# Kernel optimization log

Measured on AMD Instinct MI355X. Metric: run time of the kernel, lower is better.

Reference implementation:

```python
import jax, jax.numpy as jnp
import numpy as np

E = 8       # num experts
D = 768     # embed_dim
H = 12      # num heads
F = 3072    # expert hidden = 4*D
TOPK = 2


def setup_inputs() -> dict:
    key = jax.random.key(0)
    ks = jax.random.split(key, 8)
    B, S = 4, 1024
    s = lambda d: 1.0 / np.sqrt(d)
    return {
        "x": jax.random.normal(ks[0], (B, S, D), jnp.float32),
        "w_qkv": jax.random.normal(ks[1], (D, 3 * D), jnp.float32) * s(D),
        "b_qkv": jnp.zeros((3 * D,), jnp.float32),
        "w_o": jax.random.normal(ks[2], (D, D), jnp.float32) * s(D),
        "b_o": jnp.zeros((D,), jnp.float32),
        "w_router": jax.random.normal(ks[3], (D, E), jnp.float32) * s(D),
        "w1": jax.random.normal(ks[4], (E, D, F), jnp.float32) * s(D),
        "b1": jnp.zeros((E, F), jnp.float32),
        "w2": jax.random.normal(ks[5], (E, F, D), jnp.float32) * s(F),
        "b2": jnp.zeros((E, D), jnp.float32),
    }


def reference(x, w_qkv, b_qkv, w_o, b_o, w_router, w1, b1, w2, b2):
    B, S, Dm = x.shape
    hd = Dm // H
    # --- multi-head self-attention ---
    qkv = x @ w_qkv + b_qkv                                  # [B,S,3D]
    q, k, v = jnp.split(qkv, 3, axis=-1)
    resh = lambda t: t.reshape(B, S, H, hd).transpose(0, 2, 1, 3)  # [B,H,S,hd]
    q, k, v = resh(q), resh(k), resh(v)
    scores = jnp.einsum('bhqd,bhkd->bhqk', q, k) / np.sqrt(hd).astype(np.float32)
    attn = jax.nn.softmax(scores, axis=-1)
    ctx = jnp.einsum('bhqk,bhkd->bhqd', attn, v)
    ctx = ctx.transpose(0, 2, 1, 3).reshape(B, S, Dm)
    y = ctx @ w_o + b_o                                      # [B,S,D]
    # --- top-k MoE feed-forward ---
    t = y.reshape(B * S, Dm)                                 # [T,D]
    logits = t @ w_router                                    # [T,E]
    probs = jax.nn.softmax(logits, axis=-1)
    topv, topi = jax.lax.top_k(probs, TOPK)                  # [T,K]
    topw = topv / jnp.sum(topv, axis=-1, keepdims=True)      # renormalized gates
    T = t.shape[0]
    wfull = jnp.zeros_like(probs).at[jnp.arange(T)[:, None], topi].set(topw)  # [T,E]
    # dense all-expert compute, weighted combine (faithful to routed math)
    h = jax.nn.gelu(jnp.einsum('td,edf->etf', t, w1) + b1[:, None, :])  # [E,T,F]
    oe = jnp.einsum('etf,efd->etd', h, w2) + b2[:, None, :]              # [E,T,D]
    out = jnp.einsum('te,etd->td', wfull, oe).reshape(B, S, Dm)
    diagnostics = probs  # router probabilities as diagnostics
    return (out, diagnostics)
```

## Files before the change

### kernel.cpp

```cpp
#include <hip/hip_runtime.h>
#include <hip/hip_bf16.h>
#include <cstdint>
#include <cmath>

#define T_TOK 4096
#define DIM   768
#define HEADS 12
#define HD    64
#define NEXP  8
#define FDIM  3072

typedef __attribute__((ext_vector_type(8))) short short8v;
typedef __attribute__((ext_vector_type(4))) float float4v;

__device__ __forceinline__ float gelu_tanh(float x) {
  float u = 0.7978845608028654f * (x + 0.044715f * x * x * x);
  return 0.5f * x * (1.0f + tanhf(u));
}

__device__ __forceinline__ short f2bf(float x) {
  __hip_bfloat16 h = __float2bfloat16(x);
  return *reinterpret_cast<short*>(&h);
}

template<int TBM, int TBN>
__global__ __launch_bounds__(256) void gemm_f32(
    const float* __restrict__ A, const float* __restrict__ W,
    const float* __restrict__ bias, float* __restrict__ C,
    int M, int N, int K)
{
  constexpr int MM = TBM / 16;
  constexpr int MN = TBN / 16;
  constexpr int ALOAD = TBM * 16 / 256;
  constexpr int BLOAD = TBN * 16 / 256;
  __shared__ float As[16][TBM + 4];
  __shared__ float Bs[16][TBN + 4];
  const int bm = blockIdx.y * TBM;
  const int bn = blockIdx.x * TBN;
  const int tid = threadIdx.x;
  const int tr = tid >> 4;
  const int tc = tid & 15;

  float acc[MM][MN] = {};

  for (int k0 = 0; k0 < K; k0 += 16) {
    #pragma unroll
    for (int i = 0; i < ALOAD; i++) {
      int idx = tid + i * 256;
      int m  = idx >> 4;
      int kk = idx & 15;
      As[kk][m] = A[(size_t)(bm + m) * K + k0 + kk];
    }
    #pragma unroll
    for (int i = 0; i < BLOAD; i++) {
      int idx = tid + i * 256;
      int kk = idx / TBN;
      int n  = idx % TBN;
      Bs[kk][n] = W[(size_t)(k0 + kk) * N + bn + n];
    }
    __syncthreads();
    #pragma unroll
    for (int kk = 0; kk < 16; kk++) {
      float a[MM], b[MN];
      #pragma unroll
      for (int u4 = 0; u4 < MM / 4; u4++) {
        float4 t = *(const float4*)&As[kk][tr * MM + u4 * 4];
        a[u4*4+0]=t.x; a[u4*4+1]=t.y; a[u4*4+2]=t.z; a[u4*4+3]=t.w;
      }
      #pragma unroll
      for (int v4 = 0; v4 < MN / 4; v4++) {
        float4 t = *(const float4*)&Bs[kk][tc * MN + v4 * 4];
        b[v4*4+0]=t.x; b[v4*4+1]=t.y; b[v4*4+2]=t.z; b[v4*4+3]=t.w;
      }
      #pragma unroll
      for (int u = 0; u < MM; u++)
        #pragma unroll
        for (int v = 0; v < MN; v++)
          acc[u][v] = fmaf(a[u], b[v], acc[u][v]);
    }
    __syncthreads();
  }

  #pragma unroll
  for (int u = 0; u < MM; u++) {
    int row = bm + tr * MM + u;
    #pragma unroll
    for (int v4 = 0; v4 < MN / 4; v4++) {
      int col = bn + tc * MN + v4 * 4;
      float4 o;
      o.x = acc[u][v4*4+0] + bias[col+0];
      o.y = acc[u][v4*4+1] + bias[col+1];
      o.z = acc[u][v4*4+2] + bias[col+2];
      o.w = acc[u][v4*4+3] + bias[col+3];
      *(float4*)&C[(size_t)row * N + col] = o;
    }
  }
}

__global__ __launch_bounds__(256) void transpose_bf16(
    const float* __restrict__ W, short* __restrict__ WT, int K, int N)
{
  __shared__ float t[32][33];
  const size_t mat = (size_t)K * N;
  const float* Wp = W + blockIdx.z * mat;
  short* WTp = WT + blockIdx.z * mat;
  int n0 = blockIdx.x * 32, k0 = blockIdx.y * 32;
  int tx = threadIdx.x, ty = threadIdx.y;
  #pragma unroll
  for (int i = 0; i < 4; i++)
    t[ty + i * 8][tx] = Wp[(size_t)(k0 + ty + i * 8) * N + n0 + tx];
  __syncthreads();
  #pragma unroll
  for (int i = 0; i < 4; i++)
    WTp[(size_t)(n0 + ty + i * 8) * K + k0 + tx] = f2bf(t[tx][ty + i * 8]);
}

__global__ __launch_bounds__(256) void y2bf_kernel(
    const float* __restrict__ y, short* __restrict__ ybf)
{
  int g = blockIdx.x * 256 + threadIdx.x;
  float4 v = *(const float4*)&y[(size_t)g * 4];
  short4 s = make_short4(f2bf(v.x), f2bf(v.y), f2bf(v.z), f2bf(v.w));
  *(short4*)&ybf[(size_t)g * 4] = s;
}

__global__ __launch_bounds__(256) void moe_up(
    const short* __restrict__ ybf, const short* __restrict__ WT,
    const float* __restrict__ bias, short* __restrict__ hbuf,
    const int* __restrict__ offsets, const int* __restrict__ perm)
{
  const int e = blockIdx.z;
  const int start = offsets[e];
  const int M = offsets[e + 1] - start;
  const int bm = blockIdx.y * 128;
  if (bm >= M) return;
  const int bn = blockIdx.x * 128;

  __shared__ short As[4][128][8];
  __shared__ short Bs[4][128][8];
  __shared__ int   perm_s[128];

  const int tid  = threadIdx.x;
  const int lane = tid & 63;
  const int wave = tid >> 6;
  const int wm = wave >> 1, wn = wave & 1;
  const int lr = lane & 15;
  const int kb = lane >> 4;

  const short* WTe = WT + (size_t)e * ((size_t)FDIM * DIM);
  const float* be  = bias + (size_t)e * FDIM;

  if (tid < 128) {
    int rr = bm + tid;
    perm_s[tid] = (rr < M) ? perm[start + rr] : perm[start];
  }
  __syncthreads();

  const int q = tid & 3;
  const int mrow = tid >> 2;
  const short* aptr[2];
  const short* bptr[2];
  #pragma unroll
  for (int i = 0; i < 2; i++) {
    aptr[i] = ybf + (size_t)perm_s[mrow + i * 64] * DIM;
    bptr[i] = WTe + (size_t)(bn + mrow + i * 64) * DIM;
  }

  float4v acc[4][4] = {};

  for (int k0 = 0; k0 < DIM; k0 += 32) {
    int4 av[2], bv[2];
    #pragma unroll
    for (int i = 0; i < 2; i++) {
      av[i] = *(const int4*)(aptr[i] + k0 + q * 8);
      bv[i] = *(const int4*)(bptr[i] + k0 + q * 8);
    }
    __syncthreads();
    #pragma unroll
    for (int i = 0; i < 2; i++) {
      *(int4*)&As[q][mrow + i * 64][0] = av[i];
      *(int4*)&Bs[q][mrow + i * 64][0] = bv[i];
    }
    __syncthreads();

    short8v af[4], bfv[4];
    #pragma unroll
    for (int mi = 0; mi < 4; mi++)
      af[mi] = *(const short8v*)&As[kb][wm * 64 + mi * 16 + lr][0];
    #pragma unroll
    for (int ni = 0; ni < 4; ni++)
      bfv[ni] = *(const short8v*)&Bs[kb][wn * 64 + ni * 16 + lr][0];
    #pragma unroll
    for (int mi = 0; mi < 4; mi++)
      #pragma unroll
      for (int ni = 0; ni < 4; ni++)
        acc[mi][ni] = __builtin_amdgcn_mfma_f32_16x16x32_bf16(
            af[mi], bfv[ni], acc[mi][ni], 0, 0, 0);
  }

  #pragma unroll
  for (int ni = 0; ni < 4; ni++) {
    int col = bn + wn * 64 + ni * 16 + lr;
    float b = be[col];
    #pragma unroll
    for (int mi = 0; mi < 4; mi++) {
      int lrow0 = wm * 64 + mi * 16 + kb * 4;
      #pragma unroll
      for (int r = 0; r < 4; r++) {
        int rr = bm + lrow0 + r;
        if (rr < M)
          hbuf[(size_t)(start + rr) * FDIM + col] = f2bf(gelu_tanh(acc[mi][ni][r] + b));
      }
    }
  }
}

__global__ __launch_bounds__(256) void moe_down(
    const short* __restrict__ hbuf, const short* __restrict__ WT,
    const float* __restrict__ bias, float* __restrict__ oe,
    const int* __restrict__ offsets)
{
  const int e = blockIdx.z;
  const int start = offsets[e];
  const int M = offsets[e + 1] - start;
  const int bm = blockIdx.y * 64;
  if (bm >= M) return;
  const int bn = blockIdx.x * 128;

  __shared__ short As[4][64][8];
  __shared__ short Bs[4][128][8];

  const int tid  = threadIdx.x;
  const int lane = tid & 63;
  const int wn   = tid >> 6;
  const int lr   = lane & 15;
  const int kb   = lane >> 4;

  const short* WTe = WT + (size_t)e * ((size_t)DIM * FDIM);
  const float* be  = bias + (size_t)e * DIM;

  const int q = tid & 3;
  const int mrow = tid >> 2;
  int rr0 = bm + mrow; if (rr0 >= M) rr0 = M - 1;
  const short* aptr = hbuf + (size_t)(start + rr0) * FDIM;
  const short* bptr[2];
  #pragma unroll
  for (int i = 0; i < 2; i++)
    bptr[i] = WTe + (size_t)(bn + mrow + i * 64) * FDIM;

  float4v acc[4][2] = {};

  for (int k0 = 0; k0 < FDIM; k0 += 32) {
    int4 av = *(const int4*)(aptr + k0 + q * 8);
    int4 bv[2];
    #pragma unroll
    for (int i = 0; i < 2; i++) bv[i] = *(const int4*)(bptr[i] + k0 + q * 8);
    __syncthreads();
    *(int4*)&As[q][mrow][0] = av;
    #pragma unroll
    for (int i = 0; i < 2; i++) *(int4*)&Bs[q][mrow + i * 64][0] = bv[i];
    __syncthreads();

    short8v af[4], bfv[2];
    #pragma unroll
    for (int mi = 0; mi < 4; mi++)
      af[mi] = *(const short8v*)&As[kb][mi * 16 + lr][0];
    #pragma unroll
    for (int ni = 0; ni < 2; ni++)
      bfv[ni] = *(const short8v*)&Bs[kb][wn * 32 + ni * 16 + lr][0];
    #pragma unroll
    for (int mi = 0; mi < 4; mi++)
      #pragma unroll
      for (int ni = 0; ni < 2; ni++)
        acc[mi][ni] = __builtin_amdgcn_mfma_f32_16x16x32_bf16(
            af[mi], bfv[ni], acc[mi][ni], 0, 0, 0);
  }

  #pragma unroll
  for (int ni = 0; ni < 2; ni++) {
    int col = bn + wn * 32 + ni * 16 + lr;
    float b = be[col];
    #pragma unroll
    for (int mi = 0; mi < 4; mi++) {
      #pragma unroll
      for (int r = 0; r < 4; r++) {
        int rr = bm + mi * 16 + kb * 4 + r;
        if (rr < M)
          oe[(size_t)(start + rr) * DIM + col] = acc[mi][ni][r] + b;
      }
    }
  }
}

__global__ __launch_bounds__(256) void combine_kernel(
    const float* __restrict__ oe, const int* __restrict__ ppos,
    const float* __restrict__ topg, float* __restrict__ out)
{
  int g = blockIdx.x * 256 + threadIdx.x;
  int t = g / 192;
  int c = (g - t * 192) * 4;
  int p0 = ppos[2 * t], p1 = ppos[2 * t + 1];
  float g0 = topg[2 * t], g1 = topg[2 * t + 1];
  float4 a = *(const float4*)&oe[(size_t)p0 * DIM + c];
  float4 b = *(const float4*)&oe[(size_t)p1 * DIM + c];
  float4 o;
  o.x = g0 * a.x + g1 * b.x;
  o.y = g0 * a.y + g1 * b.y;
  o.z = g0 * a.z + g1 * b.z;
  o.w = g0 * a.w + g1 * b.w;
  *(float4*)&out[(size_t)t * DIM + c] = o;
}

__global__ __launch_bounds__(256) void attn_kernel(
    const float* __restrict__ qkv, float* __restrict__ ctx)
{
  const int qt = blockIdx.x;
  const int bh = blockIdx.y;
  const int b = bh / HEADS, h = bh % HEADS;
  const float* base = qkv + (size_t)b * 1024 * (3 * DIM) + h * 64;

  __shared__ float ks[64][64];
  __shared__ float vs[64][64];

  const int tid   = threadIdx.x;
  const int wv    = tid >> 6;
  const int qhalf = wv & 1;
  const int khalf = wv >> 1;
  const int lane  = tid & 63;
  const int grp   = lane >> 2;
  const int sub   = lane & 3;
  const int q0    = qhalf * 32 + grp * 2;
  const int dpart = sub * 16;

  const float qscale = 0.125f * 1.44269504088896f;
  float qA[16], qB[16], accA[16] = {}, accB[16] = {};
  float lA = 0.f, lB = 0.f;

  {
    const float* qpA = base + (size_t)(qt * 64 + q0) * (3 * DIM) + dpart;
    const float* qpB = qpA + 3 * DIM;
    #pragma unroll
    for (int d4 = 0; d4 < 4; d4++) {
      float4 ta = *(const float4*)(qpA + d4 * 4);
      float4 tb = *(const float4*)(qpB + d4 * 4);
      qA[d4*4+0]=ta.x*qscale; qA[d4*4+1]=ta.y*qscale; qA[d4*4+2]=ta.z*qscale; qA[d4*4+3]=ta.w*qscale;
      qB[d4*4+0]=tb.x*qscale; qB[d4*4+1]=tb.y*qscale; qB[d4*4+2]=tb.z*qscale; qB[d4*4+3]=tb.w*qscale;
    }
  }

  for (int kt = 0; kt < 16; kt++) {
    __syncthreads();
    #pragma unroll
    for (int i = 0; i < 4; i++) {
      int idx = tid + i * 256;
      int r = idx >> 4, c4 = idx & 15;
      const float* kp = base + (size_t)(kt * 64 + r) * (3 * DIM) + c4 * 4;
      *(float4*)&ks[r][c4 * 4] = *(const float4*)(kp + DIM);
      *(float4*)&vs[r][c4 * 4] = *(const float4*)(kp + 2 * DIM);
    }
    __syncthreads();

    #pragma unroll 2
    for (int jj = 0; jj < 32; jj++) {
      int j = khalf * 32 + jj;
      float4 k0v = *(const float4*)&ks[j][dpart];
      float4 k1v = *(const float4*)&ks[j][dpart + 4];
      float4 k2v = *(const float4*)&ks[j][dpart + 8];
      float4 k3v = *(const float4*)&ks[j][dpart + 12];
      float kr[16] = {k0v.x,k0v.y,k0v.z,k0v.w, k1v.x,k1v.y,k1v.z,k1v.w,
                      k2v.x,k2v.y,k2v.z,k2v.w, k3v.x,k3v.y,k3v.z,k3v.w};
      float sA = 0.f, sB = 0.f;
      #pragma unroll
      for (int d = 0; d < 16; d++) {
        sA = fmaf(qA[d], kr[d], sA);
        sB = fmaf(qB[d], kr[d], sB);
      }
      sA += __shfl_xor(sA, 1);  sB += __shfl_xor(sB, 1);
      sA += __shfl_xor(sA, 2);  sB += __shfl_xor(sB, 2);
      float pA = exp2f(sA);
      float pB = exp2f(sB);
      lA += pA;  lB += pB;
      float4 v0v = *(const float4*)&vs[j][dpart];
      float4 v1v = *(const float4*)&vs[j][dpart + 4];
      float4 v2v = *(const float4*)&vs[j][dpart + 8];
      float4 v3v = *(const float4*)&vs[j][dpart + 12];
      float vr[16] = {v0v.x,v0v.y,v0v.z,v0v.w, v1v.x,v1v.y,v1v.z,v1v.w,
                      v2v.x,v2v.y,v2v.z,v2v.w, v3v.x,v3v.y,v3v.z,v3v.w};
      #pragma unroll
      for (int d = 0; d < 16; d++) {
        accA[d] = fmaf(pA, vr[d], accA[d]);
        accB[d] = fmaf(pB, vr[d], accB[d]);
      }
    }
  }

  __syncthreads();
  if (khalf == 1) {
    #pragma unroll
    for (int d4 = 0; d4 < 4; d4++) {
      *(float4*)&ks[q0][dpart + d4*4] =
          make_float4(accA[d4*4], accA[d4*4+1], accA[d4*4+2], accA[d4*4+3]);
      *(float4*)&ks[q0 + 1][dpart + d4*4] =
          make_float4(accB[d4*4], accB[d4*4+1], accB[d4*4+2], accB[d4*4+3]);
    }
    if (sub == 0) { vs[0][q0] = lA; vs[0][q0 + 1] = lB; }
  }
  __syncthreads();
  if (khalf == 0) {
    lA += vs[0][q0];
    lB += vs[0][q0 + 1];
    float invA = 1.f / lA, invB = 1.f / lB;
    float* opA = ctx + ((size_t)b * 1024 + qt * 64 + q0) * DIM + h * 64 + dpart;
    float* opB = opA + DIM;
    #pragma unroll
    for (int d4 = 0; d4 < 4; d4++) {
      float4 ca = *(const float4*)&ks[q0][dpart + d4*4];
      float4 cb = *(const float4*)&ks[q0 + 1][dpart + d4*4];
      float4 oa, ob;
      oa.x = (accA[d4*4+0] + ca.x) * invA;
      oa.y = (accA[d4*4+1] + ca.y) * invA;
      oa.z = (accA[d4*4+2] + ca.z) * invA;
      oa.w = (accA[d4*4+3] + ca.w) * invA;
      ob.x = (accB[d4*4+0] + cb.x) * invB;
      ob.y = (accB[d4*4+1] + cb.y) * invB;
      ob.z = (accB[d4*4+2] + cb.z) * invB;
      ob.w = (accB[d4*4+3] + cb.w) * invB;
      *(float4*)(opA + d4 * 4) = oa;
      *(float4*)(opB + d4 * 4) = ob;
    }
  }
}

__global__ __launch_bounds__(256) void router_kernel(
    const float* __restrict__ y, const float* __restrict__ wr,
    float* __restrict__ probs, int* __restrict__ topi,
    float* __restrict__ topg, int* __restrict__ counts)
{
  __shared__ float w[DIM * NEXP];
  const int tid = threadIdx.x;
  for (int i = tid; i < DIM * NEXP; i += 256) w[i] = wr[i];
  __syncthreads();

  const int t = blockIdx.x * 256 + tid;
  const float* yp = y + (size_t)t * DIM;
  float logit[8] = {};
  for (int d = 0; d < DIM; d++) {
    float xv = yp[d];
    #pragma unroll
    for (int e = 0; e < 8; e++) logit[e] = fmaf(xv, w[d * 8 + e], logit[e]);
  }
  float mx = logit[0];
  #pragma unroll
  for (int e = 1; e < 8; e++) mx = fmaxf(mx, logit[e]);
  float p[8], sum = 0.f;
  #pragma unroll
  for (int e = 0; e < 8; e++) { p[e] = __expf(logit[e] - mx); sum += p[e]; }
  float inv = 1.f / sum;
  #pragma unroll
  for (int e = 0; e < 8; e++) { p[e] *= inv; probs[(size_t)t * 8 + e] = p[e]; }

  int i0 = 0;
  #pragma unroll
  for (int e = 1; e < 8; e++) if (p[e] > p[i0]) i0 = e;
  int i1 = (i0 == 0) ? 1 : 0;
  #pragma unroll
  for (int e = 0; e < 8; e++) if (e != i0 && p[e] > p[i1]) i1 = e;
  float g = p[i0] + p[i1];
  topi[2 * t] = i0;  topi[2 * t + 1] = i1;
  topg[2 * t] = p[i0] / g;  topg[2 * t + 1] = p[i1] / g;
  atomicAdd(&counts[i0], 1);
  atomicAdd(&counts[i1], 1);
}

__global__ void init_meta(int* counts) {
  if (threadIdx.x < 8) counts[threadIdx.x] = 0;
}

__global__ void scan_kernel(const int* __restrict__ counts,
                            int* __restrict__ offsets, int* __restrict__ cursors) {
  if (threadIdx.x == 0) {
    int s = 0;
    for (int e = 0; e < 8; e++) { offsets[e] = s; cursors[e] = s; s += counts[e]; }
    offsets[8] = s;
  }
}

__global__ __launch_bounds__(256) void scatter_kernel(
    const int* __restrict__ topi, int* __restrict__ cursors,
    int* __restrict__ perm, int* __restrict__ ppos)
{
  const int t = blockIdx.x * 256 + threadIdx.x;
  #pragma unroll
  for (int s = 0; s < 2; s++) {
    int e = topi[2 * t + s];
    int pos = atomicAdd(&cursors[e], 1);
    perm[pos] = t;
    ppos[2 * t + s] = pos;
  }
}

extern "C" void kernel_launch(void* const* d_in, const int* in_sizes, int n_in,
                              void* d_out, int out_size, void* d_ws, size_t ws_size,
                              hipStream_t stream) {
  const float* x        = (const float*)d_in[0];
  const float* w_qkv    = (const float*)d_in[1];
  const float* b_qkv    = (const float*)d_in[2];
  const float* w_o      = (const float*)d_in[3];
  const float* b_o      = (const float*)d_in[4];
  const float* w_router = (const float*)d_in[5];
  const float* w1       = (const float*)d_in[6];
  const float* b1       = (const float*)d_in[7];
  const float* w2       = (const float*)d_in[8];
  const float* b2       = (const float*)d_in[9];

  float* out   = (float*)d_out;
  float* probs = out + (size_t)T_TOK * DIM;

  char* ws = (char*)d_ws;
  float* qkv  = (float*)ws;
  short* hbuf = (short*)ws;
  short* wT   = (short*)(ws + 50331648);
  float* ctx  = (float*)(ws + 88080384);
  short* ybf  = (short*)(ws + 88080384);
  float* oe   = (float*)(ws + 88080384);
  float* y    = (float*)(ws + 100663296);
  char*  meta = ws + 113246208;
  int*   counts  = (int*)meta;
  int*   cursors = counts + 8;
  int*   offsets = cursors + 8;
  int*   topi    = offsets + 16;
  float* topg    = (float*)(topi + 8192);
  int*   perm    = (int*)(topg + 8192);
  int*   ppos    = perm + 8192;

  init_meta<<<1, 64, 0, stream>>>(counts);

  gemm_f32<128, 64><<<dim3((3 * DIM) / 64, T_TOK / 128), 256, 0, stream>>>(
      x, w_qkv, b_qkv, qkv, T_TOK, 3 * DIM, DIM);

  attn_kernel<<<dim3(16, 48), 256, 0, stream>>>(qkv, ctx);

  gemm_f32<64, 64><<<dim3(DIM / 64, T_TOK / 64), 256, 0, stream>>>(
      ctx, w_o, b_o, y, T_TOK, DIM, DIM);

  router_kernel<<<16, 256, 0, stream>>>(y, w_router, probs, topi, topg, counts);
  scan_kernel<<<1, 64, 0, stream>>>(counts, offsets, cursors);
  scatter_kernel<<<16, 256, 0, stream>>>(topi, cursors, perm, ppos);

  y2bf_kernel<<<(T_TOK * DIM / 4) / 256, 256, 0, stream>>>(y, ybf);

  transpose_bf16<<<dim3(FDIM / 32, DIM / 32, NEXP), dim3(32, 8), 0, stream>>>(
      w1, wT, DIM, FDIM);
  moe_up<<<dim3(FDIM / 128, T_TOK / 128, NEXP), 256, 0, stream>>>(
      ybf, wT, b1, hbuf, offsets, perm);

  transpose_bf16<<<dim3(DIM / 32, FDIM / 32, NEXP), dim3(32, 8), 0, stream>>>(
      w2, wT, FDIM, DIM);
  moe_down<<<dim3(DIM / 128, T_TOK / 64, NEXP), 256, 0, stream>>>(
      hbuf, wT, b2, oe, offsets);

  combine_kernel<<<(T_TOK * DIM / 4) / 256, 256, 0, stream>>>(oe, ppos, topg, out);
}
```

Before: 1.138 ms.

## Register-prefetch next tiles in fp32 GEMM and attention, retile attention threads

The fp32 GEMM now loads A and W tiles as float4 into registers one k-step ahead and stores them to shared memory before computing, dropping one barrier per iteration. The attention kernel likewise prefetches the next K/V tile into registers and remaps threads so each handles 4 queries over 8 head dims, trading extra shuffles for more reuse of each K/V value loaded from shared memory. The QKV GEMM tile grows to 128x128 and launch bounds request 3 blocks per SM. The aim is to hide global-load latency and cut shared-memory traffic per FMA, at the cost of more registers, which could spill or lower occupancy.

```diff
diff --git a/kernel.cpp b/kernel.cpp
--- a/kernel.cpp
+++ b/kernel.cpp
@@ -24,15 +24,15 @@
 }
 
 template<int TBM, int TBN>
-__global__ __launch_bounds__(256) void gemm_f32(
+__global__ __launch_bounds__(256, 3) void gemm_f32(
     const float* __restrict__ A, const float* __restrict__ W,
     const float* __restrict__ bias, float* __restrict__ C,
     int M, int N, int K)
 {
   constexpr int MM = TBM / 16;
   constexpr int MN = TBN / 16;
-  constexpr int ALOAD = TBM * 16 / 256;
-  constexpr int BLOAD = TBN * 16 / 256;
+  constexpr int ALOADS = TBM * 4 / 256;
+  constexpr int BLOADS = TBN * 4 / 256;
   __shared__ float As[16][TBM + 4];
   __shared__ float Bs[16][TBN + 4];
   const int bm = blockIdx.y * TBM;
@@ -42,21 +42,51 @@
   const int tc = tid & 15;
 
   float acc[MM][MN] = {};
+  float4 areg[ALOADS], breg[BLOADS];
+
+  #pragma unroll
+  for (int i = 0; i < ALOADS; i++) {
+    int fidx = tid + i * 256;
+    int row = fidx >> 2, c4 = fidx & 3;
+    areg[i] = *(const float4*)&A[(size_t)(bm + row) * K + c4 * 4];
+  }
+  #pragma unroll
+  for (int i = 0; i < BLOADS; i++) {
+    int fidx = tid + i * 256;
+    int kk = fidx / (TBN / 4), n4 = fidx % (TBN / 4);
+    breg[i] = *(const float4*)&W[(size_t)kk * N + bn + n4 * 4];
+  }
 
   for (int k0 = 0; k0 < K; k0 += 16) {
-    #pragma unroll
-    for (int i = 0; i < ALOAD; i++) {
-      int idx = tid + i * 256;
-      int m  = idx >> 4;
-      int kk = idx & 15;
-      As[kk][m] = A[(size_t)(bm + m) * K + k0 + kk];
-    }
-    #pragma unroll
-    for (int i = 0; i < BLOAD; i++) {
-      int idx = tid + i * 256;
-      int kk = idx / TBN;
-      int n  = idx % TBN;
-      Bs[kk][n] = W[(size_t)(k0 + kk) * N + bn + n];
+    __syncthreads();
+    #pragma unroll
+    for (int i = 0; i < ALOADS; i++) {
+      int fidx = tid + i * 256;
+      int row = fidx >> 2, c4 = fidx & 3;
+      As[c4 * 4 + 0][row] = areg[i].x;
+      As[c4 * 4 + 1][row] = areg[i].y;
+      As[c4 * 4 + 2][row] = areg[i].z;
+      As[c4 * 4 + 3][row] = areg[i].w;
+    }
+    #pragma unroll
+    for (int i = 0; i < BLOADS; i++) {
+      int fidx = tid + i * 256;
+      int kk = fidx / (TBN / 4), n4 = fidx % (TBN / 4);
+      *(float4*)&Bs[kk][n4 * 4] = breg[i];
+    }
+    if (k0 + 16 < K) {
+      #pragma unroll
+      for (int i = 0; i < ALOADS; i++) {
+        int fidx = tid + i * 256;
+        int row = fidx >> 2, c4 = fidx & 3;
+        areg[i] = *(const float4*)&A[(size_t)(bm + row) * K + k0 + 16 + c4 * 4];
+      }
+      #pragma unroll
+      for (int i = 0; i < BLOADS; i++) {
+        int fidx = tid + i * 256;
+        int kk = fidx / (TBN / 4), n4 = fidx % (TBN / 4);
+        breg[i] = *(const float4*)&W[(size_t)(k0 + 16 + kk) * N + bn + n4 * 4];
+      }
     }
     __syncthreads();
     #pragma unroll
@@ -78,7 +108,6 @@
         for (int v = 0; v < MN; v++)
           acc[u][v] = fmaf(a[u], b[v], acc[u][v]);
     }
-    __syncthreads();
   }
 
   #pragma unroll
@@ -311,7 +340,7 @@
   *(float4*)&out[(size_t)t * DIM + c] = o;
 }
 
-__global__ __launch_bounds__(256) void attn_kernel(
+__global__ __launch_bounds__(256, 3) void attn_kernel(
     const float* __restrict__ qkv, float* __restrict__ ctx)
 {
   const int qt = blockIdx.x;
@@ -319,33 +348,40 @@
   const int b = bh / HEADS, h = bh % HEADS;
   const float* base = qkv + (size_t)b * 1024 * (3 * DIM) + h * 64;
 
-  __shared__ float ks[64][64];
-  __shared__ float vs[64][64];
+  __shared__ float ks[64 * 64];
+  __shared__ float vs[64 * 64];
+  __shared__ float lred[2][32];
 
   const int tid   = threadIdx.x;
   const int wv    = tid >> 6;
   const int qhalf = wv & 1;
   const int khalf = wv >> 1;
   const int lane  = tid & 63;
-  const int grp   = lane >> 2;
-  const int sub   = lane & 3;
-  const int q0    = qhalf * 32 + grp * 2;
-  const int dpart = sub * 16;
+  const int grp   = lane >> 3;
+  const int sub   = lane & 7;
+  const int dpart = sub * 8;
+  const int qbase = qhalf * 32 + grp * 4;
 
   const float qscale = 0.125f * 1.44269504088896f;
-  float qA[16], qB[16], accA[16] = {}, accB[16] = {};
-  float lA = 0.f, lB = 0.f;
-
-  {
-    const float* qpA = base + (size_t)(qt * 64 + q0) * (3 * DIM) + dpart;
-    const float* qpB = qpA + 3 * DIM;
-    #pragma unroll
-    for (int d4 = 0; d4 < 4; d4++) {
-      float4 ta = *(const float4*)(qpA + d4 * 4);
-      float4 tb = *(const float4*)(qpB + d4 * 4);
-      qA[d4*4+0]=ta.x*qscale; qA[d4*4+1]=ta.y*qscale; qA[d4*4+2]=ta.z*qscale; qA[d4*4+3]=ta.w*qscale;
-      qB[d4*4+0]=tb.x*qscale; qB[d4*4+1]=tb.y*qscale; qB[d4*4+2]=tb.z*qscale; qB[d4*4+3]=tb.w*qscale;
-    }
+  float q[4][8], acc[4][8] = {}, l[4] = {0.f, 0.f, 0.f, 0.f};
+
+  #pragma unroll
+  for (int i = 0; i < 4; i++) {
+    const float* qp = base + (size_t)(qt * 64 + qbase + i) * (3 * DIM) + dpart;
+    float4 t0 = *(const float4*)qp;
+    float4 t1 = *(const float4*)(qp + 4);
+    q[i][0]=t0.x*qscale; q[i][1]=t0.y*qscale; q[i][2]=t0.z*qscale; q[i][3]=t0.w*qscale;
+    q[i][4]=t1.x*qscale; q[i][5]=t1.y*qscale; q[i][6]=t1.z*qscale; q[i][7]=t1.w*qscale;
+  }
+
+  float4 kreg[4], vreg[4];
+  #pragma unroll
+  for (int i = 0; i < 4; i++) {
+    int idx = tid + i * 256;
+    int r = idx >> 4, c4 = idx & 15;
+    const float* kp = base + (size_t)r * (3 * DIM) + c4 * 4;
+    kreg[i] = *(const float4*)(kp + DIM);
+    vreg[i] = *(const float4*)(kp + 2 * DIM);
   }
 
   for (int kt = 0; kt < 16; kt++) {
@@ -354,79 +390,98 @@
     for (int i = 0; i < 4; i++) {
       int idx = tid + i * 256;
       int r = idx >> 4, c4 = idx & 15;
-      const float* kp = base + (size_t)(kt * 64 + r) * (3 * DIM) + c4 * 4;
-      *(float4*)&ks[r][c4 * 4] = *(const float4*)(kp + DIM);
-      *(float4*)&vs[r][c4 * 4] = *(const float4*)(kp + 2 * DIM);
+      *(float4*)&ks[r * 64 + c4 * 4] = kreg[i];
+      *(float4*)&vs[r * 64 + c4 * 4] = vreg[i];
+    }
+    if (kt < 15) {
+      #pragma unroll
+      for (int i = 0; i < 4; i++) {
+        int idx = tid + i * 256;
+        int r = idx >> 4, c4 = idx & 15;
+        const float* kp = base + (size_t)((kt + 1) * 64 + r) * (3 * DIM) + c4 * 4;
+        kreg[i] = *(const float4*)(kp + DIM);
+        vreg[i] = *(const float4*)(kp + 2 * DIM);
+      }
     }
     __syncthreads();
 
     #pragma unroll 2
     for (int jj = 0; jj < 32; jj++) {
       int j = khalf * 32 + jj;
-      float4 k0v = *(const float4*)&ks[j][dpart];
-      float4 k1v = *(const float4*)&ks[j][dpart + 4];
-      float4 k2v = *(const float4*)&ks[j][dpart + 8];
-      float4 k3v = *(const float4*)&ks[j][dpart + 12];
-      float kr[16] = {k0v.x,k0v.y,k0v.z,k0v.w, k1v.x,k1v.y,k1v.z,k1v.w,
-                      k2v.x,k2v.y,k2v.z,k2v.w, k3v.x,k3v.y,k3v.z,k3v.w};
-      float sA = 0.f, sB = 0.f;
-      #pragma unroll
-      for (int d = 0; d < 16; d++) {
-        sA = fmaf(qA[d], kr[d], sA);
-        sB = fmaf(qB[d], kr[d], sB);
-      }
-      sA += __shfl_xor(sA, 1);  sB += __shfl_xor(sB, 1);
-      sA += __shfl_xor(sA, 2);  sB += __shfl_xor(sB, 2);
-      float pA = exp2f(sA);
-      float pB = exp2f(sB);
-      lA += pA;  lB += pB;
-      float4 v0v = *(const float4*)&vs[j][dpart];
-      float4 v1v = *(const float4*)&vs[j][dpart + 4];
-      float4 v2v = *(const float4*)&vs[j][dpart + 8];
-      float4 v3v = *(const float4*)&vs[j][dpart + 12];
-      float vr[16] = {v0v.x,v0v.y,v0v.z,v0v.w, v1v.x,v1v.y,v1v.z,v1v.w,
-                      v2v.x,v2v.y,v2v.z,v2v.w, v3v.x,v3v.y,v3v.z,v3v.w};
-      #pragma unroll
-      for (int d = 0; d < 16; d++) {
-        accA[d] = fmaf(pA, vr[d], accA[d]);
-        accB[d] = fmaf(pB, vr[d], accB[d]);
+      float4 k0v = *(const float4*)&ks[j * 64 + dpart];
+      float4 k1v = *(const float4*)&ks[j * 64 + dpart + 4];
+      float kr[8] = {k0v.x,k0v.y,k0v.z,k0v.w, k1v.x,k1v.y,k1v.z,k1v.w};
+      float s0 = 0.f, s1 = 0.f, s2 = 0.f, s3 = 0.f;
+      #pragma unroll
+      for (int d = 0; d < 8; d++) {
+        s0 = fmaf(q[0][d], kr[d], s0);
+        s1 = fmaf(q[1][d], kr[d], s1);
+        s2 = fmaf(q[2][d], kr[d], s2);
+        s3 = fmaf(q[3][d], kr[d], s3);
+      }
+      s0 += __shfl_xor(s0, 1); s1 += __shfl_xor(s1, 1);
+      s2 += __shfl_xor(s2, 1); s3 += __shfl_xor(s3, 1);
+      s0 += __shfl_xor(s0, 2); s1 += __shfl_xor(s1, 2);
+      s2 += __shfl_xor(s2, 2); s3 += __shfl_xor(s3, 2);
+      s0 += __shfl_xor(s0, 4); s1 += __shfl_xor(s1, 4);
+      s2 += __shfl_xor(s2, 4); s3 += __shfl_xor(s3, 4);
+      float p0 = exp2f(s0), p1 = exp2f(s1), p2 = exp2f(s2), p3 = exp2f(s3);
+      l[0] += p0; l[1] += p1; l[2] += p2; l[3] += p3;
+      float4 v0v = *(const float4*)&vs[j * 64 + dpart];
+      float4 v1v = *(const float4*)&vs[j * 64 + dpart + 4];
+      float vr[8] = {v0v.x,v0v.y,v0v.z,v0v.w, v1v.x,v1v.y,v1v.z,v1v.w};
+      #pragma unroll
+      for (int d = 0; d < 8; d++) {
+        acc[0][d] = fmaf(p0, vr[d], acc[0][d]);
+        acc[1][d] = fmaf(p1, vr[d], acc[1][d]);
+        acc[2][d] = fmaf(p2, vr[d], acc[2][d]);
+        acc[3][d] = fmaf(p3, vr[d], acc[3][d]);
       }
     }
   }
 
   __syncthreads();
+  float* bufA = ks;
+  float* bufB = vs;
   if (khalf == 1) {
-    #pragma unroll
-    for (int d4 = 0; d4 < 4; d4++) {
-      *(float4*)&ks[q0][dpart + d4*4] =
-          make_float4(accA[d4*4], accA[d4*4+1], accA[d4*4+2], accA[d4*4+3]);
-      *(float4*)&ks[q0 + 1][dpart + d4*4] =
-          make_float4(accB[d4*4], accB[d4*4+1], accB[d4*4+2], accB[d4*4+3]);
-    }
-    if (sub == 0) { vs[0][q0] = lA; vs[0][q0 + 1] = lB; }
+    float* buf = qhalf ? bufB : bufA;
+    #pragma unroll
+    for (int i = 0; i < 4; i++) {
+      #pragma unroll
+      for (int d4 = 0; d4 < 2; d4++) {
+        int idx4 = i * 2 + d4;
+        *(float4*)&buf[(idx4 * 64 + lane) * 4] =
+            make_float4(acc[i][d4*4+0], acc[i][d4*4+1], acc[i][d4*4+2], acc[i][d4*4+3]);
+      }
+    }
+    if (sub == 0) {
+      #pragma unroll
+      for (int i = 0; i < 4; i++) lred[qhalf][grp * 4 + i] = l[i];
+    }
   }
   __syncthreads();
   if (khalf == 0) {
-    lA += vs[0][q0];
-    lB += vs[0][q0 + 1];
-    float invA = 1.f / lA, invB = 1.f / lB;
-    float* opA = ctx + ((size_t)b * 1024 + qt * 64 + q0) * DIM + h * 64 + dpart;
-    float* opB = opA + DIM;
-    #pragma unroll
-    for (int d4 = 0; d4 < 4; d4++) {
-      float4 ca = *(const float4*)&ks[q0][dpart + d4*4];
-      float4 cb = *(const float4*)&ks[q0 + 1][dpart + d4*4];
-      float4 oa, ob;
-      oa.x = (accA[d4*4+0] + ca.x) * invA;
-      oa.y = (accA[d4*4+1] + ca.y) * invA;
-      oa.z = (accA[d4*4+2] + ca.z) * invA;
-      oa.w = (accA[d4*4+3] + ca.w) * invA;
-      ob.x = (accB[d4*4+0] + cb.x) * invB;
-      ob.y = (accB[d4*4+1] + cb.y) * invB;
-      ob.z = (accB[d4*4+2] + cb.z) * invB;
-      ob.w = (accB[d4*4+3] + cb.w) * invB;
-      *(float4*)(opA + d4 * 4) = oa;
-      *(float4*)(opB + d4 * 4) = ob;
+    const float* buf = qhalf ? bufB : bufA;
+    #pragma unroll
+    for (int i = 0; i < 4; i++) {
+      #pragma unroll
+      for (int d4 = 0; d4 < 2; d4++) {
+        int idx4 = i * 2 + d4;
+        float4 t = *(const float4*)&buf[(idx4 * 64 + lane) * 4];
+        acc[i][d4*4+0] += t.x; acc[i][d4*4+1] += t.y;
+        acc[i][d4*4+2] += t.z; acc[i][d4*4+3] += t.w;
+      }
+      l[i] += lred[qhalf][grp * 4 + i];
+    }
+    #pragma unroll
+    for (int i = 0; i < 4; i++) {
+      float inv = 1.f / l[i];
+      float* op = ctx + ((size_t)b * 1024 + qt * 64 + qbase + i) * DIM + h * 64 + dpart;
+      float4 o0, o1;
+      o0.x = acc[i][0]*inv; o0.y = acc[i][1]*inv; o0.z = acc[i][2]*inv; o0.w = acc[i][3]*inv;
+      o1.x = acc[i][4]*inv; o1.y = acc[i][5]*inv; o1.z = acc[i][6]*inv; o1.w = acc[i][7]*inv;
+      *(float4*)op = o0;
+      *(float4*)(op + 4) = o1;
     }
   }
 }
@@ -535,7 +590,7 @@
 
   init_meta<<<1, 64, 0, stream>>>(counts);
 
-  gemm_f32<128, 64><<<dim3((3 * DIM) / 64, T_TOK / 128), 256, 0, stream>>>(
+  gemm_f32<128, 128><<<dim3((3 * DIM) / 128, T_TOK / 128), 256, 0, stream>>>(
       x, w_qkv, b_qkv, qkv, T_TOK, 3 * DIM, DIM);
 
   attn_kernel<<<dim3(16, 48), 256, 0, stream>>>(qkv, ctx);
```

Result: slower. 1.317 ms (+15.7%).
